# Kernel tuning notes

Hardware: AMD Instinct MI355X
Metric: run time of the kernel (lower is better)

## Reference

```python
import jax, jax.numpy as jnp
import numpy as np
from jax import lax

TAU = 0.1
N_ITERS = 20
B, N = 2048, 256


def setup_inputs() -> dict:
    key = jax.random.key(0)
    k1, k2 = jax.random.split(key)
    x = jax.random.normal(k1, (B, N), dtype=jnp.float32)
    x_norm = jax.random.normal(k2, (B, N), dtype=jnp.float32)
    reference_vec = jnp.linspace(-1.0, 1.0, N, dtype=jnp.float32)
    return {"x": x, "x_norm": x_norm, "reference_vec": reference_vec}


def reference(x, x_norm, reference_vec):
    # log_alpha: [B, N, N] = -|x_norm_i - ref_j| / tau
    log_alpha = -jnp.abs(x_norm[..., None] - reference_vec) / TAU

    def body(la, _):
        la = la - jax.nn.logsumexp(la, axis=-1, keepdims=True)  # row norm
        la = la - jax.nn.logsumexp(la, axis=-2, keepdims=True)  # col norm
        return la, None

    log_alpha, _ = lax.scan(body, log_alpha, None, length=N_ITERS)
    perm = jnp.exp(log_alpha)  # soft permutation [B, N, N]
    return jnp.einsum("bij,bj->bi", perm, x)
```

## Files before the change

kernel.cpp:

```cpp
#include <hip/hip_runtime.h>

#define NN 256
#define NITER 20
static constexpr float KK = 14.426950408889634f;

template<int CTRL, int RM>
__device__ __forceinline__ float dppadd(float x) {
  int v = __builtin_amdgcn_update_dpp(0, __float_as_int(x), CTRL, RM, 0xF, true);
  return x + __int_as_float(v);
}
template<int CTRL, int RM>
__device__ __forceinline__ int dppaddi(int x) {
  int v = __builtin_amdgcn_update_dpp(0, x, CTRL, RM, 0xF, true);
  return x + v;
}
__device__ __forceinline__ float rlane(float v, int l) {
  return __int_as_float(__builtin_amdgcn_readlane(__float_as_int(v), l));
}
__device__ __forceinline__ float rcpf(float x) {
  float r; asm("v_rcp_f32 %0, %1" : "=v"(r) : "v"(x)); return r;
}
__device__ __forceinline__ int swz(int s) { return s + (s >> 4); }

__global__ __launch_bounds__(64)
void sinkhorn_wave(const float* __restrict__ x,
                   const float* __restrict__ xn,
                   const float* __restrict__ refv,
                   float* __restrict__ out)
{
  __shared__ __align__(16) float2   W[274];
  __shared__ __align__(16) unsigned hist[NN];
  __shared__ __align__(16) int      exclArr[NN];
  __shared__ __align__(16) float    xsArr[NN];
  __shared__ __align__(16) int      origArr[NN];

  const int lane = threadIdx.x;
  const int b = blockIdx.x;
  const int j4 = lane * 4;
  const size_t base = (size_t)b * NN;

  float xnv[4], xv[4], rv[4];
  { float4 t = *(const float4*)(xn + base + j4); xnv[0]=t.x; xnv[1]=t.y; xnv[2]=t.z; xnv[3]=t.w; }
  { float4 t = *(const float4*)(x  + base + j4); xv[0]=t.x;  xv[1]=t.y;  xv[2]=t.z;  xv[3]=t.w; }
  { float4 t = *(const float4*)(refv + j4);      rv[0]=t.x;  rv[1]=t.y;  rv[2]=t.z;  rv[3]=t.w; }

  *(uint4*)&hist[j4] = make_uint4(0u, 0u, 0u, 0u);
  float vc[4]; int cb[4]; unsigned rtn[4];
  #pragma unroll
  for (int t = 0; t < 4; ++t) {
    vc[t] = fminf(fmaxf(xnv[t], -1.0f), 1.0f);
    cb[t] = (int)fmaf(vc[t], 127.5f, 127.5f);
    rtn[t] = atomicAdd(&hist[cb[t]], 1u);
  }
  uint4 hv = *(uint4*)&hist[j4];
  int ih0 = (int)hv.x, ih1 = ih0 + (int)hv.y, ih2 = ih1 + (int)hv.z, ih3 = ih2 + (int)hv.w;
  int sH = ih3;
  sH = dppaddi<0x111,0xF>(sH); sH = dppaddi<0x112,0xF>(sH);
  sH = dppaddi<0x114,0xF>(sH); sH = dppaddi<0x118,0xF>(sH);
  sH = dppaddi<0x142,0xA>(sH); sH = dppaddi<0x143,0xC>(sH);
  const int offH = sH - ih3;
  int slotM[4] = { offH, offH + ih0, offH + ih1, offH + ih2 };
  *(int4*)&exclArr[j4] = make_int4(slotM[0], slotM[1], slotM[2], slotM[3]);
  #pragma unroll
  for (int t = 0; t < 4; ++t) {
    int slot = exclArr[cb[t]] + (int)rtn[t];
    xsArr[slot]   = vc[t];
    origArr[slot] = j4 + t;
  }
  float xs[4]; int orig[4];
  { float4 t = *(float4*)&xsArr[j4]; xs[0]=t.x; xs[1]=t.y; xs[2]=t.z; xs[3]=t.w; }
  { int4  t = *(int4*)&origArr[j4]; orig[0]=t.x; orig[1]=t.y; orig[2]=t.z; orig[3]=t.w; }

  int slotJ[4];
  #pragma unroll
  for (int t = 0; t < 4; ++t) {
    slotJ[t] = swz((int)fmaf(xs[t], 127.5f, 127.5f) + 1);
    slotM[t] = swz(slotM[t]);
  }

  float Ep[4], Em[4], Epx[4], Emx[4];
  #pragma unroll
  for (int t = 0; t < 4; ++t) {
    Ep[t]  = exp2f( KK * rv[t]);  Em[t]  = exp2f(-KK * rv[t]);
    Epx[t] = exp2f( KK * xs[t]);  Emx[t] = exp2f(-KK * xs[t]);
  }

  const int wbase = swz(j4);
  auto scan_store = [&](float pa0, float pa1, float pa2, float pa3,
                        float qb0, float qb1, float qb2, float qb3) {
    float ip0 = pa0, ip1 = ip0 + pa1, ip2 = ip1 + pa2, ip3 = ip2 + pa3;
    float sq3 = qb3, sq2 = sq3 + qb2, sq1 = sq2 + qb1, sq0 = sq1 + qb0;
    float sP = ip3;
    sP = dppadd<0x111,0xF>(sP); sP = dppadd<0x112,0xF>(sP);
    sP = dppadd<0x114,0xF>(sP); sP = dppadd<0x118,0xF>(sP);
    sP = dppadd<0x142,0xA>(sP); sP = dppadd<0x143,0xC>(sP);
    float offP = sP - ip3;
    float sQ = sq0;
    sQ = dppadd<0x101,0xF>(sQ); sQ = dppadd<0x102,0xF>(sQ);
    sQ = dppadd<0x104,0xF>(sQ); sQ = dppadd<0x108,0xF>(sQ);
    float q1 = rlane(sQ, 16), q2 = rlane(sQ, 32), q3 = rlane(sQ, 48);
    int row = lane >> 4;
    float offQ = sQ - sq0;
    offQ += (row < 1) ? q1 : 0.f;
    offQ += (row < 2) ? q2 : 0.f;
    offQ += (row < 3) ? q3 : 0.f;
    float4 w0 = make_float4(offP,       offQ + sq0, offP + ip0, offQ + sq1);
    float4 w1 = make_float4(offP + ip1, offQ + sq2, offP + ip2, offQ + sq3);
    *(float4*)&W[wbase]     = w0;
    *(float4*)&W[wbase + 2] = w1;
    if (lane == 63) W[272] = make_float2(sP, 0.f);
  };

  float vC[4] = {1.f, 1.f, 1.f, 1.f}, vR[4];
  #pragma unroll 1
  for (int it = 0; it < NITER; ++it) {
    scan_store(Ep[0]*vC[0], Ep[1]*vC[1], Ep[2]*vC[2], Ep[3]*vC[3],
               Em[0]*vC[0], Em[1]*vC[1], Em[2]*vC[2], Em[3]*vC[3]);
    #pragma unroll
    for (int t = 0; t < 4; ++t) {
      float2 w = W[slotJ[t]];
      vR[t] = rcpf(fmaf(Emx[t], w.x, Epx[t] * w.y));
    }
    scan_store(Epx[0]*vR[0], Epx[1]*vR[1], Epx[2]*vR[2], Epx[3]*vR[3],
               Emx[0]*vR[0], Emx[1]*vR[1], Emx[2]*vR[2], Emx[3]*vR[3]);
    float vCo0 = vC[0], vCo1 = vC[1], vCo2 = vC[2], vCo3 = vC[3];
    #pragma unroll
    for (int t = 0; t < 4; ++t) {
      float2 w = W[slotM[t]];
      vC[t] = rcpf(fmaf(Em[t], w.x, Ep[t] * w.y));
    }
    if (it >= 6) {
      bool ok = (fabsf(vC[0] - vCo0) <= 1e-6f * vC[0]) &&
                (fabsf(vC[1] - vCo1) <= 1e-6f * vC[1]) &&
                (fabsf(vC[2] - vCo2) <= 1e-6f * vC[2]) &&
                (fabsf(vC[3] - vCo3) <= 1e-6f * vC[3]);
      if (__all(ok)) break;
    }
  }
  {
    float g0 = vC[0]*xv[0], g1 = vC[1]*xv[1], g2 = vC[2]*xv[2], g3 = vC[3]*xv[3];
    scan_store(Ep[0]*g0, Ep[1]*g1, Ep[2]*g2, Ep[3]*g3,
               Em[0]*g0, Em[1]*g1, Em[2]*g2, Em[3]*g3);
    #pragma unroll
    for (int t = 0; t < 4; ++t) {
      float2 w = W[slotJ[t]];
      float S = fmaf(Emx[t], w.x, Epx[t] * w.y);
      xsArr[orig[t]] = vR[t] * S;
    }
    float4 o = *(float4*)&xsArr[j4];
    *(float4*)(out + base + j4) = o;
  }
}

extern "C" void kernel_launch(void* const* d_in, const int* in_sizes, int n_in,
                              void* d_out, int out_size, void* d_ws, size_t ws_size,
                              hipStream_t stream) {
  const float* x    = (const float*)d_in[0];
  const float* xnrm = (const float*)d_in[1];
  const float* refv = (const float*)d_in[2];
  float* out = (float*)d_out;
  const int B = in_sizes[0] / NN;
  sinkhorn_wave<<<dim3(B), dim3(64), 0, stream>>>(x, xnrm, refv, out);
}
```

Baseline: 21.45 us.

## Pack prefix/suffix scans into float2 vectors and drop early-exit convergence check

The forward prefix and reverse suffix scans in scan_store are packed into 2-wide float vectors, pairing the suffix operands in reversed order, so the multiplies and adds can map to packed FP32 instructions. The early-exit convergence test is removed, so all 20 Sinkhorn iterations always run. That drops the per-iteration compare and wave vote, but gives up the ability to stop early once the scalings have converged.

```diff
diff --git a/kernel.cpp b/kernel.cpp
--- a/kernel.cpp
+++ b/kernel.cpp
@@ -3,6 +3,8 @@
 #define NN 256
 #define NITER 20
 static constexpr float KK = 14.426950408889634f;
+
+typedef float v2f __attribute__((ext_vector_type(2)));
 
 template<int CTRL, int RM>
 __device__ __forceinline__ float dppadd(float x) {
@@ -84,28 +86,34 @@
     Ep[t]  = exp2f( KK * rv[t]);  Em[t]  = exp2f(-KK * rv[t]);
     Epx[t] = exp2f( KK * xs[t]);  Emx[t] = exp2f(-KK * xs[t]);
   }
+  v2f E2r[4], E2c[4];
+  #pragma unroll
+  for (int t = 0; t < 4; ++t) {
+    E2r[t] = (v2f){Ep[t],  Em[3 - t]};
+    E2c[t] = (v2f){Epx[t], Emx[3 - t]};
+  }
 
   const int wbase = swz(j4);
-  auto scan_store = [&](float pa0, float pa1, float pa2, float pa3,
-                        float qb0, float qb1, float qb2, float qb3) {
-    float ip0 = pa0, ip1 = ip0 + pa1, ip2 = ip1 + pa2, ip3 = ip2 + pa3;
-    float sq3 = qb3, sq2 = sq3 + qb2, sq1 = sq2 + qb1, sq0 = sq1 + qb0;
-    float sP = ip3;
+  auto scan_store = [&](v2f z0, v2f z1, v2f z2, v2f z3) {
+    v2f s1 = z0 + z1;
+    v2f s2 = s1 + z2;
+    v2f s3 = s2 + z3;
+    float sP = s3.x;
     sP = dppadd<0x111,0xF>(sP); sP = dppadd<0x112,0xF>(sP);
     sP = dppadd<0x114,0xF>(sP); sP = dppadd<0x118,0xF>(sP);
     sP = dppadd<0x142,0xA>(sP); sP = dppadd<0x143,0xC>(sP);
-    float offP = sP - ip3;
-    float sQ = sq0;
+    float offP = sP - s3.x;
+    float sQ = s3.y;
     sQ = dppadd<0x101,0xF>(sQ); sQ = dppadd<0x102,0xF>(sQ);
     sQ = dppadd<0x104,0xF>(sQ); sQ = dppadd<0x108,0xF>(sQ);
     float q1 = rlane(sQ, 16), q2 = rlane(sQ, 32), q3 = rlane(sQ, 48);
     int row = lane >> 4;
-    float offQ = sQ - sq0;
+    float offQ = sQ - s3.y;
     offQ += (row < 1) ? q1 : 0.f;
     offQ += (row < 2) ? q2 : 0.f;
     offQ += (row < 3) ? q3 : 0.f;
-    float4 w0 = make_float4(offP,       offQ + sq0, offP + ip0, offQ + sq1);
-    float4 w1 = make_float4(offP + ip1, offQ + sq2, offP + ip2, offQ + sq3);
+    float4 w0 = make_float4(offP,        offQ + s3.y, offP + z0.x, offQ + s2.y);
+    float4 w1 = make_float4(offP + s1.x, offQ + s1.y, offP + s2.x, offQ + z0.y);
     *(float4*)&W[wbase]     = w0;
     *(float4*)&W[wbase + 2] = w1;
     if (lane == 63) W[272] = make_float2(sP, 0.f);
@@ -114,33 +122,31 @@
   float vC[4] = {1.f, 1.f, 1.f, 1.f}, vR[4];
   #pragma unroll 1
   for (int it = 0; it < NITER; ++it) {
-    scan_store(Ep[0]*vC[0], Ep[1]*vC[1], Ep[2]*vC[2], Ep[3]*vC[3],
-               Em[0]*vC[0], Em[1]*vC[1], Em[2]*vC[2], Em[3]*vC[3]);
+    scan_store(E2r[0] * (v2f){vC[0], vC[3]},
+               E2r[1] * (v2f){vC[1], vC[2]},
+               E2r[2] * (v2f){vC[2], vC[1]},
+               E2r[3] * (v2f){vC[3], vC[0]});
     #pragma unroll
     for (int t = 0; t < 4; ++t) {
       float2 w = W[slotJ[t]];
       vR[t] = rcpf(fmaf(Emx[t], w.x, Epx[t] * w.y));
     }
-    scan_store(Epx[0]*vR[0], Epx[1]*vR[1], Epx[2]*vR[2], Epx[3]*vR[3],
-               Emx[0]*vR[0], Emx[1]*vR[1], Emx[2]*vR[2], Emx[3]*vR[3]);
-    float vCo0 = vC[0], vCo1 = vC[1], vCo2 = vC[2], vCo3 = vC[3];
+    scan_store(E2c[0] * (v2f){vR[0], vR[3]},
+               E2c[1] * (v2f){vR[1], vR[2]},
+               E2c[2] * (v2f){vR[2], vR[1]},
+               E2c[3] * (v2f){vR[3], vR[0]});
     #pragma unroll
     for (int t = 0; t < 4; ++t) {
       float2 w = W[slotM[t]];
       vC[t] = rcpf(fmaf(Em[t], w.x, Ep[t] * w.y));
     }
-    if (it >= 6) {
-      bool ok = (fabsf(vC[0] - vCo0) <= 1e-6f * vC[0]) &&
-                (fabsf(vC[1] - vCo1) <= 1e-6f * vC[1]) &&
-                (fabsf(vC[2] - vCo2) <= 1e-6f * vC[2]) &&
-                (fabsf(vC[3] - vCo3) <= 1e-6f * vC[3]);
-      if (__all(ok)) break;
-    }
   }
   {
     float g0 = vC[0]*xv[0], g1 = vC[1]*xv[1], g2 = vC[2]*xv[2], g3 = vC[3]*xv[3];
-    scan_store(Ep[0]*g0, Ep[1]*g1, Ep[2]*g2, Ep[3]*g3,
-               Em[0]*g0, Em[1]*g1, Em[2]*g2, Em[3]*g3);
+    scan_store(E2r[0] * (v2f){g0, g3},
+               E2r[1] * (v2f){g1, g2},
+               E2r[2] * (v2f){g2, g1},
+               E2r[3] * (v2f){g3, g0});
     #pragma unroll
     for (int t = 0; t < 4; ++t) {
       float2 w = W[slotJ[t]];
```

After: 19.52 us. 1.1x faster.

## Split each Sinkhorn row across two cooperating wavefronts with cross-wave scan totals

Applied to the files above, without the earlier changes.

Each batch row is now handled by a 128-thread block of two wavefronts, each owning 2 of the 256 elements per thread instead of 4. Each wave runs its own DPP prefix and suffix scan, then combines the halves through a few shared totals and mask-weighted adds. This shortens the serial chain of work each wave does per Sinkhorn half-step. In exchange it adds a block barrier at every half-iteration. It also drops the convergence early-exit, so all 20 iterations always run.

```diff
diff --git a/kernel.cpp b/kernel.cpp
--- a/kernel.cpp
+++ b/kernel.cpp
@@ -3,6 +3,8 @@
 #define NN 256
 #define NITER 20
 static constexpr float KK = 14.426950408889634f;
+
+typedef float v2f __attribute__((ext_vector_type(2)));
 
 template<int CTRL, int RM>
 __device__ __forceinline__ float dppadd(float x) {
@@ -21,134 +23,161 @@
   float r; asm("v_rcp_f32 %0, %1" : "=v"(r) : "v"(x)); return r;
 }
 __device__ __forceinline__ int swz(int s) { return s + (s >> 4); }
+__device__ __forceinline__ float wscanP(float t) {
+  float s = t;
+  s = dppadd<0x111,0xF>(s); s = dppadd<0x112,0xF>(s);
+  s = dppadd<0x114,0xF>(s); s = dppadd<0x118,0xF>(s);
+  s = dppadd<0x142,0xA>(s); s = dppadd<0x143,0xC>(s);
+  return s;
+}
+__device__ __forceinline__ float wscanS(float t) {
+  float s = t;
+  s = dppadd<0x101,0xF>(s); s = dppadd<0x102,0xF>(s);
+  s = dppadd<0x104,0xF>(s); s = dppadd<0x108,0xF>(s);
+  return s;
+}
 
-__global__ __launch_bounds__(64)
-void sinkhorn_wave(const float* __restrict__ x,
+__global__ __launch_bounds__(128)
+void sinkhorn_team(const float* __restrict__ x,
                    const float* __restrict__ xn,
                    const float* __restrict__ refv,
                    float* __restrict__ out)
 {
-  __shared__ __align__(16) float2   W[274];
+  __shared__ __align__(16) float2   WA[274];
+  __shared__ __align__(16) float2   WB[274];
+  __shared__ __align__(16) float    TTa[4];
+  __shared__ __align__(16) float    TTb[4];
   __shared__ __align__(16) unsigned hist[NN];
   __shared__ __align__(16) int      exclArr[NN];
   __shared__ __align__(16) float    xsArr[NN];
-  __shared__ __align__(16) int      origArr[NN];
+  __shared__ __align__(16) int      ogArr[NN];
 
-  const int lane = threadIdx.x;
-  const int b = blockIdx.x;
-  const int j4 = lane * 4;
-  const size_t base = (size_t)b * NN;
+  const int tid  = threadIdx.x;
+  const int lane = tid & 63;
+  const int wid  = tid >> 6;
+  const int row  = lane >> 4;
+  const int s0   = tid * 2;
+  const size_t base = (size_t)blockIdx.x * NN;
 
-  float xnv[4], xv[4], rv[4];
-  { float4 t = *(const float4*)(xn + base + j4); xnv[0]=t.x; xnv[1]=t.y; xnv[2]=t.z; xnv[3]=t.w; }
-  { float4 t = *(const float4*)(x  + base + j4); xv[0]=t.x;  xv[1]=t.y;  xv[2]=t.z;  xv[3]=t.w; }
-  { float4 t = *(const float4*)(refv + j4);      rv[0]=t.x;  rv[1]=t.y;  rv[2]=t.z;  rv[3]=t.w; }
+  float2 xn2 = *(const float2*)(xn + base + s0);
+  float2 xv2 = *(const float2*)(x  + base + s0);
+  float2 rv2 = *(const float2*)(refv + s0);
 
-  *(uint4*)&hist[j4] = make_uint4(0u, 0u, 0u, 0u);
-  float vc[4]; int cb[4]; unsigned rtn[4];
-  #pragma unroll
-  for (int t = 0; t < 4; ++t) {
-    vc[t] = fminf(fmaxf(xnv[t], -1.0f), 1.0f);
-    cb[t] = (int)fmaf(vc[t], 127.5f, 127.5f);
-    rtn[t] = atomicAdd(&hist[cb[t]], 1u);
+  *(uint2*)&hist[s0] = make_uint2(0u, 0u);
+  __syncthreads();
+  float vc0 = fminf(fmaxf(xn2.x, -1.0f), 1.0f);
+  float vc1 = fminf(fmaxf(xn2.y, -1.0f), 1.0f);
+  int cb0 = (int)fmaf(vc0, 127.5f, 127.5f);
+  int cb1 = (int)fmaf(vc1, 127.5f, 127.5f);
+  unsigned rtn0 = atomicAdd(&hist[cb0], 1u);
+  unsigned rtn1 = atomicAdd(&hist[cb1], 1u);
+  __syncthreads();
+  {
+    uint4 hv = *(uint4*)&hist[4 * lane];
+    int ih0 = (int)hv.x, ih1 = ih0 + (int)hv.y, ih2 = ih1 + (int)hv.z, ih3 = ih2 + (int)hv.w;
+    int sH = ih3;
+    sH = dppaddi<0x111,0xF>(sH); sH = dppaddi<0x112,0xF>(sH);
+    sH = dppaddi<0x114,0xF>(sH); sH = dppaddi<0x118,0xF>(sH);
+    sH = dppaddi<0x142,0xA>(sH); sH = dppaddi<0x143,0xC>(sH);
+    const int offH = sH - ih3;
+    *(int4*)&exclArr[4 * lane] = make_int4(offH, offH + ih0, offH + ih1, offH + ih2);
   }
-  uint4 hv = *(uint4*)&hist[j4];
-  int ih0 = (int)hv.x, ih1 = ih0 + (int)hv.y, ih2 = ih1 + (int)hv.z, ih3 = ih2 + (int)hv.w;
-  int sH = ih3;
-  sH = dppaddi<0x111,0xF>(sH); sH = dppaddi<0x112,0xF>(sH);
-  sH = dppaddi<0x114,0xF>(sH); sH = dppaddi<0x118,0xF>(sH);
-  sH = dppaddi<0x142,0xA>(sH); sH = dppaddi<0x143,0xC>(sH);
-  const int offH = sH - ih3;
-  int slotM[4] = { offH, offH + ih0, offH + ih1, offH + ih2 };
-  *(int4*)&exclArr[j4] = make_int4(slotM[0], slotM[1], slotM[2], slotM[3]);
-  #pragma unroll
-  for (int t = 0; t < 4; ++t) {
-    int slot = exclArr[cb[t]] + (int)rtn[t];
-    xsArr[slot]   = vc[t];
-    origArr[slot] = j4 + t;
+  {
+    int sa = exclArr[cb0] + (int)rtn0;
+    int sb = exclArr[cb1] + (int)rtn1;
+    xsArr[sa] = vc0;  ogArr[sa] = s0;
+    xsArr[sb] = vc1;  ogArr[sb] = s0 + 1;
   }
-  float xs[4]; int orig[4];
-  { float4 t = *(float4*)&xsArr[j4]; xs[0]=t.x; xs[1]=t.y; xs[2]=t.z; xs[3]=t.w; }
-  { int4  t = *(int4*)&origArr[j4]; orig[0]=t.x; orig[1]=t.y; orig[2]=t.z; orig[3]=t.w; }
+  __syncthreads();
+  float2 xs2 = *(float2*)&xsArr[s0];
+  int2   og2 = *(int2*)&ogArr[s0];
+  int2   ex2 = *(int2*)&exclArr[s0];
 
-  int slotJ[4];
-  #pragma unroll
-  for (int t = 0; t < 4; ++t) {
-    slotJ[t] = swz((int)fmaf(xs[t], 127.5f, 127.5f) + 1);
-    slotM[t] = swz(slotM[t]);
+  int rJ0 = (int)fmaf(xs2.x, 127.5f, 127.5f) + 1;
+  int rJ1 = (int)fmaf(xs2.y, 127.5f, 127.5f) + 1;
+  const float mJh0 = (rJ0 >= 128) ? 1.f : 0.f, mJl0 = 1.f - mJh0;
+  const float mJh1 = (rJ1 >= 128) ? 1.f : 0.f, mJl1 = 1.f - mJh1;
+  const float mMh0 = (ex2.x >= 128) ? 1.f : 0.f, mMl0 = 1.f - mMh0;
+  const float mMh1 = (ex2.y >= 128) ? 1.f : 0.f, mMl1 = 1.f - mMh1;
+  const int sJ0 = swz(rJ0), sJ1 = swz(rJ1);
+  const int sM0 = swz(ex2.x), sM1 = swz(ex2.y);
+  const int sw0 = swz(s0), sw1 = swz(s0 + 1);
+
+  const float Ep0  = exp2f( KK * rv2.x), Ep1  = exp2f( KK * rv2.y);
+  const float Em0  = exp2f(-KK * rv2.x), Em1  = exp2f(-KK * rv2.y);
+  const float Epx0 = exp2f( KK * xs2.x), Epx1 = exp2f( KK * xs2.y);
+  const float Emx0 = exp2f(-KK * xs2.x), Emx1 = exp2f(-KK * xs2.y);
+  const v2f E2r0 = (v2f){Ep0,  Em1},  E2r1 = (v2f){Ep1,  Em0};
+  const v2f E2c0 = (v2f){Epx0, Emx1}, E2c1 = (v2f){Epx1, Emx0};
+  const float mk1 = (row < 1) ? 1.f : 0.f;
+  const float mk2 = (row < 2) ? 1.f : 0.f;
+  const float mk3 = (row < 3) ? 1.f : 0.f;
+
+  auto scan_store = [&](float2* W_, float* TT_, v2f z0, v2f z1) {
+    v2f s1v = z0 + z1;
+    float sP = wscanP(s1v.x);
+    float offP = sP - s1v.x;
+    float sQ = wscanS(s1v.y);
+    float q1 = rlane(sQ, 16), q2 = rlane(sQ, 32), q3 = rlane(sQ, 48);
+    float offQ = sQ - s1v.y;
+    offQ = fmaf(mk1, q1, offQ);
+    offQ = fmaf(mk2, q2, offQ);
+    offQ = fmaf(mk3, q3, offQ);
+    W_[sw0] = make_float2(offP,        offQ + s1v.y);
+    W_[sw1] = make_float2(offP + z0.x, offQ + z0.y);
+    if (lane == 63) {
+      TT_[wid * 2] = sP;
+      if (wid == 1) W_[272] = make_float2(sP, 0.f);
+    }
+    if (lane == 0) TT_[wid * 2 + 1] = offQ + s1v.y;
+  };
+
+  float vC0 = 1.f, vC1 = 1.f, vR0, vR1;
+  #pragma unroll 1
+  for (int it = 0; it < NITER; ++it) {
+    scan_store(WA, TTa, E2r0 * (v2f){vC0, vC1}, E2r1 * (v2f){vC1, vC0});
+    __syncthreads();
+    {
+      float4 tt = *(float4*)&TTa[0];
+      float Tp0 = tt.x, Tq1 = tt.w;
+      float2 wa = WA[sJ0];
+      float2 wb = WA[sJ1];
+      float P0 = fmaf(mJh0, Tp0, wa.x), Q0 = fmaf(mJl0, Tq1, wa.y);
+      float P1 = fmaf(mJh1, Tp0, wb.x), Q1 = fmaf(mJl1, Tq1, wb.y);
+      vR0 = rcpf(fmaf(Emx0, P0, Epx0 * Q0));
+      vR1 = rcpf(fmaf(Emx1, P1, Epx1 * Q1));
+    }
+    scan_store(WB, TTb, E2c0 * (v2f){vR0, vR1}, E2c1 * (v2f){vR1, vR0});
+    __syncthreads();
+    {
+      float4 tt = *(float4*)&TTb[0];
+      float Tp0 = tt.x, Tq1 = tt.w;
+      float2 wa = WB[sM0];
+      float2 wb = WB[sM1];
+      float P0 = fmaf(mMh0, Tp0, wa.x), Q0 = fmaf(mMl0, Tq1, wa.y);
+      float P1 = fmaf(mMh1, Tp0, wb.x), Q1 = fmaf(mMl1, Tq1, wb.y);
+      vC0 = rcpf(fmaf(Em0, P0, Ep0 * Q0));
+      vC1 = rcpf(fmaf(Em1, P1, Ep1 * Q1));
+    }
   }
 
-  float Ep[4], Em[4], Epx[4], Emx[4];
-  #pragma unroll
-  for (int t = 0; t < 4; ++t) {
-    Ep[t]  = exp2f( KK * rv[t]);  Em[t]  = exp2f(-KK * rv[t]);
-    Epx[t] = exp2f( KK * xs[t]);  Emx[t] = exp2f(-KK * xs[t]);
-  }
-
-  const int wbase = swz(j4);
-  auto scan_store = [&](float pa0, float pa1, float pa2, float pa3,
-                        float qb0, float qb1, float qb2, float qb3) {
-    float ip0 = pa0, ip1 = ip0 + pa1, ip2 = ip1 + pa2, ip3 = ip2 + pa3;
-    float sq3 = qb3, sq2 = sq3 + qb2, sq1 = sq2 + qb1, sq0 = sq1 + qb0;
-    float sP = ip3;
-    sP = dppadd<0x111,0xF>(sP); sP = dppadd<0x112,0xF>(sP);
-    sP = dppadd<0x114,0xF>(sP); sP = dppadd<0x118,0xF>(sP);
-    sP = dppadd<0x142,0xA>(sP); sP = dppadd<0x143,0xC>(sP);
-    float offP = sP - ip3;
-    float sQ = sq0;
-    sQ = dppadd<0x101,0xF>(sQ); sQ = dppadd<0x102,0xF>(sQ);
-    sQ = dppadd<0x104,0xF>(sQ); sQ = dppadd<0x108,0xF>(sQ);
-    float q1 = rlane(sQ, 16), q2 = rlane(sQ, 32), q3 = rlane(sQ, 48);
-    int row = lane >> 4;
-    float offQ = sQ - sq0;
-    offQ += (row < 1) ? q1 : 0.f;
-    offQ += (row < 2) ? q2 : 0.f;
-    offQ += (row < 3) ? q3 : 0.f;
-    float4 w0 = make_float4(offP,       offQ + sq0, offP + ip0, offQ + sq1);
-    float4 w1 = make_float4(offP + ip1, offQ + sq2, offP + ip2, offQ + sq3);
-    *(float4*)&W[wbase]     = w0;
-    *(float4*)&W[wbase + 2] = w1;
-    if (lane == 63) W[272] = make_float2(sP, 0.f);
-  };
-
-  float vC[4] = {1.f, 1.f, 1.f, 1.f}, vR[4];
-  #pragma unroll 1
-  for (int it = 0; it < NITER; ++it) {
-    scan_store(Ep[0]*vC[0], Ep[1]*vC[1], Ep[2]*vC[2], Ep[3]*vC[3],
-               Em[0]*vC[0], Em[1]*vC[1], Em[2]*vC[2], Em[3]*vC[3]);
-    #pragma unroll
-    for (int t = 0; t < 4; ++t) {
-      float2 w = W[slotJ[t]];
-      vR[t] = rcpf(fmaf(Emx[t], w.x, Epx[t] * w.y));
-    }
-    scan_store(Epx[0]*vR[0], Epx[1]*vR[1], Epx[2]*vR[2], Epx[3]*vR[3],
-               Emx[0]*vR[0], Emx[1]*vR[1], Emx[2]*vR[2], Emx[3]*vR[3]);
-    float vCo0 = vC[0], vCo1 = vC[1], vCo2 = vC[2], vCo3 = vC[3];
-    #pragma unroll
-    for (int t = 0; t < 4; ++t) {
-      float2 w = W[slotM[t]];
-      vC[t] = rcpf(fmaf(Em[t], w.x, Ep[t] * w.y));
-    }
-    if (it >= 6) {
-      bool ok = (fabsf(vC[0] - vCo0) <= 1e-6f * vC[0]) &&
-                (fabsf(vC[1] - vCo1) <= 1e-6f * vC[1]) &&
-                (fabsf(vC[2] - vCo2) <= 1e-6f * vC[2]) &&
-                (fabsf(vC[3] - vCo3) <= 1e-6f * vC[3]);
-      if (__all(ok)) break;
-    }
-  }
   {
-    float g0 = vC[0]*xv[0], g1 = vC[1]*xv[1], g2 = vC[2]*xv[2], g3 = vC[3]*xv[3];
-    scan_store(Ep[0]*g0, Ep[1]*g1, Ep[2]*g2, Ep[3]*g3,
-               Em[0]*g0, Em[1]*g1, Em[2]*g2, Em[3]*g3);
-    #pragma unroll
-    for (int t = 0; t < 4; ++t) {
-      float2 w = W[slotJ[t]];
-      float S = fmaf(Emx[t], w.x, Epx[t] * w.y);
-      xsArr[orig[t]] = vR[t] * S;
-    }
-    float4 o = *(float4*)&xsArr[j4];
-    *(float4*)(out + base + j4) = o;
+    float g0 = vC0 * xv2.x, g1 = vC1 * xv2.y;
+    scan_store(WA, TTa, E2r0 * (v2f){g0, g1}, E2r1 * (v2f){g1, g0});
+    __syncthreads();
+    float4 tt = *(float4*)&TTa[0];
+    float Tp0 = tt.x, Tq1 = tt.w;
+    float2 wa = WA[sJ0];
+    float2 wb = WA[sJ1];
+    float P0 = fmaf(mJh0, Tp0, wa.x), Q0 = fmaf(mJl0, Tq1, wa.y);
+    float P1 = fmaf(mJh1, Tp0, wb.x), Q1 = fmaf(mJl1, Tq1, wb.y);
+    float S0 = fmaf(Emx0, P0, Epx0 * Q0);
+    float S1 = fmaf(Emx1, P1, Epx1 * Q1);
+    xsArr[og2.x] = vR0 * S0;
+    xsArr[og2.y] = vR1 * S1;
+    __syncthreads();
+    float2 o = *(float2*)&xsArr[s0];
+    *(float2*)(out + base + s0) = o;
   }
 }
 
@@ -160,5 +189,5 @@
   const float* refv = (const float*)d_in[2];
   float* out = (float*)d_out;
   const int B = in_sizes[0] / NN;
-  sinkhorn_wave<<<dim3(B), dim3(64), 0, stream>>>(x, xnrm, refv, out);
+  sinkhorn_team<<<dim3(B), dim3(128), 0, stream>>>(x, xnrm, refv, out);
 }
```

Result: slower. 23.77 us (+10.8%).
